# Kernel optimization log

Hardware: AMD Instinct MI355X
Metric: run time of the kernel (lower is better)

The kernel has to match this reference:

```python
import jax, jax.numpy as jnp
import numpy as np

D_MODEL = 1024
NUM_HEADS = 16
HEAD_DIM = D_MODEL // NUM_HEADS


def setup_inputs() -> dict:
    key = jax.random.key(0)
    k_x, k_wqkv, k_bqkv, k_wfc, k_bfc = jax.random.split(key, 5)
    scale_in = 1.0 / np.sqrt(D_MODEL)
    return {
        "x": jax.random.normal(k_x, (2, 2048, D_MODEL), dtype=jnp.float32),
        # torch nn.Linear stores weight as [out_features, in_features]
        "w_qkv": jax.random.uniform(k_wqkv, (3 * D_MODEL, D_MODEL), jnp.float32, -scale_in, scale_in),
        "b_qkv": jax.random.uniform(k_bqkv, (3 * D_MODEL,), jnp.float32, -scale_in, scale_in),
        "w_fc": jax.random.uniform(k_wfc, (D_MODEL, D_MODEL), jnp.float32, -scale_in, scale_in),
        "b_fc": jax.random.uniform(k_bfc, (D_MODEL,), jnp.float32, -scale_in, scale_in),
    }


def reference(x, w_qkv, b_qkv, w_fc, b_fc):
    B, S, _ = x.shape
    # fused QKV projection: [B,S,3*d_model]
    qkv = jnp.einsum("bsd,ed->bse", x, w_qkv) + b_qkv
    # [B,S,H,3*head_dim] -> [B,H,S,3*head_dim]
    qkv = qkv.reshape(B, S, NUM_HEADS, 3 * HEAD_DIM).transpose(0, 2, 1, 3)
    Q, K, V = jnp.split(qkv, 3, axis=-1)  # each [B,H,S,head_dim]
    scores = jnp.einsum("bhqd,bhkd->bhqk", Q, K) / np.sqrt(HEAD_DIM).astype(np.float32)
    attention = jax.nn.softmax(scores, axis=-1)  # [B,H,S,S]
    values = jnp.einsum("bhqk,bhkd->bhqd", attention, V)
    # [B,H,S,head_dim] -> [B,S,d_model]
    values = values.transpose(0, 2, 1, 3).reshape(B, S, D_MODEL)
    out = jnp.einsum("bsd,ed->bse", values, w_fc) + b_fc
    return out
```

## Files before the change

kernel.cpp:

```cpp
#include <hip/hip_runtime.h>
#include <hip/hip_bf16.h>
#include <hip/hip_fp16.h>

#define D_MODEL 1024
#define NH 16
#define HD 64
#define BATCH 2
#define SEQ 2048

typedef __attribute__((ext_vector_type(8))) short short8;
typedef __attribute__((ext_vector_type(4))) float floatx4;
typedef __attribute__((ext_vector_type(16))) float floatx16;
typedef __attribute__((ext_vector_type(8))) _Float16 half8;

static __device__ __forceinline__ short f2bf(float f) {
    __hip_bfloat16 h = __float2bfloat16(f);
    return *reinterpret_cast<short*>(&h);
}
static __device__ __forceinline__ unsigned int pk2bf(float a, float b) {
    float2 t; t.x = a; t.y = b;
    __hip_bfloat162 h2 = __float22bfloat162_rn(t);
    return *reinterpret_cast<unsigned int*>(&h2);
}
static __device__ __forceinline__ void pl32swap(unsigned &a, unsigned &b) {
    asm("v_permlane32_swap_b32 %0, %1" : "+v"(a), "+v"(b));
}
static __device__ __forceinline__ short8 mk8(unsigned a, unsigned b,
                                             unsigned c, unsigned d) {
    union { unsigned u[4]; short8 s; } t;
    t.u[0] = a; t.u[1] = b; t.u[2] = c; t.u[3] = d;
    return t.s;
}
static __device__ __forceinline__ float fexp2(float x) {
    return __builtin_amdgcn_exp2f(x);
}

#define GLDS(gp, lp) __builtin_amdgcn_global_load_lds( \
    (const __attribute__((address_space(1))) void*)(gp), \
    (__attribute__((address_space(3))) void*)(lp), 16, 0, 0)

__global__ __launch_bounds__(256) void cvt_all(
    const float* __restrict__ x, const float* __restrict__ wq,
    const float* __restrict__ wf,
    short* __restrict__ Xb, short* __restrict__ Wqb, short* __restrict__ Wfb)
{
    int i = blockIdx.x * 256 + threadIdx.x;
    const float* src; short* dst; int off;
    if (i < 524288)      { src = x;  dst = Xb;  off = i; }
    else if (i < 917504) { src = wq; dst = Wqb; off = i - 524288; }
    else                 { src = wf; dst = Wfb; off = i - 917504; }
    float4 a = *reinterpret_cast<const float4*>(src + off * 8);
    float4 b = *reinterpret_cast<const float4*>(src + off * 8 + 4);
    short8 o;
    o[0] = f2bf(a.x); o[1] = f2bf(a.y); o[2] = f2bf(a.z); o[3] = f2bf(a.w);
    o[4] = f2bf(b.x); o[5] = f2bf(b.y); o[6] = f2bf(b.z); o[7] = f2bf(b.w);
    *reinterpret_cast<short8*>(dst + off * 8) = o;
}

__global__ __launch_bounds__(256) void qkv_gemm(
    const short* __restrict__ X, const short* __restrict__ W,
    const float* __restrict__ bias,
    short* __restrict__ Qs, short* __restrict__ Ks, short* __restrict__ Vt_g)
{
    __shared__ __align__(16) short SH[4][128 * 32];
    const int tid = threadIdx.x;

    const int lin = blockIdx.x;
    const int g = lin & 7;
    const int loc = lin >> 3;
    const int mi = loc / 3;
    const int j3 = loc - mi * 3;
    const int m0 = mi * 128;
    const int n0 = (g + 8 * j3) * 128;
    const int bi = m0 >> 11, sl0 = m0 & 2047;

    const int w = tid >> 6, lane = tid & 63;
    const int quad = lane >> 4, l15 = lane & 15;
    const int wm2 = w >> 1, wn2 = w & 1;

    const int r1 = tid >> 2,        c1 = tid & 3;
    const int g1 = c1 ^ (r1 & 3) ^ ((r1 >> 2) & 3);
    const int r2 = (tid + 256) >> 2, c2 = tid & 3;
    const int g2 = c2 ^ (r2 & 3) ^ ((r2 >> 2) & 3);

    const short* Xs1 = X + (size_t)(m0 + r1) * 1024 + g1 * 8;
    const short* Xs2 = X + (size_t)(m0 + r2) * 1024 + g2 * 8;
    const short* Ws1 = W + (size_t)(n0 + r1) * 1024 + g1 * 8;
    const short* Ws2 = W + (size_t)(n0 + r2) * 1024 + g2 * 8;

    const int rsw = (quad ^ (l15 & 3) ^ ((l15 >> 2) & 3)) * 8;

    floatx4 acc[4][4];
#pragma unroll
    for (int i = 0; i < 4; i++)
#pragma unroll
        for (int j = 0; j < 4; j++) acc[i][j] = (floatx4)0.0f;

    GLDS(Xs1, &SH[0][tid * 8]);
    GLDS(Xs2, &SH[0][(tid + 256) * 8]);
    GLDS(Ws1, &SH[2][tid * 8]);
    GLDS(Ws2, &SH[2][(tid + 256) * 8]);
    __syncthreads();

    int cur = 0;
    for (int step = 0; step < 32; step++) {
        const int kn = (step + 1) * 32;
        GLDS(Xs1 + kn, &SH[cur ^ 1][tid * 8]);
        GLDS(Xs2 + kn, &SH[cur ^ 1][(tid + 256) * 8]);
        GLDS(Ws1 + kn, &SH[2 + (cur ^ 1)][tid * 8]);
        GLDS(Ws2 + kn, &SH[2 + (cur ^ 1)][(tid + 256) * 8]);

        const short* As = &SH[cur][0];
        const short* Bs = &SH[2 + cur][0];
        short8 a[4], b[4];
#pragma unroll
        for (int t = 0; t < 4; t++) {
            int ra = wm2 * 64 + t * 16 + l15;
            int rb = wn2 * 64 + t * 16 + l15;
            a[t] = *reinterpret_cast<const short8*>(&As[ra * 32 + rsw]);
            b[t] = *reinterpret_cast<const short8*>(&Bs[rb * 32 + rsw]);
        }
#pragma unroll
        for (int mt = 0; mt < 4; mt++)
#pragma unroll
            for (int nt = 0; nt < 4; nt++)
                acc[mt][nt] = __builtin_amdgcn_mfma_f32_16x16x32_bf16(
                    a[mt], b[nt], acc[mt][nt], 0, 0, 0);

        __syncthreads();
        cur ^= 1;
    }

    __syncthreads();
    short* EA = &SH[0][0];
    short* T  = &SH[0][0];
#pragma unroll
    for (int half = 0; half < 2; half++) {
        const int colg0 = n0 + half * 64;
        const int h = colg0 / 192;
        const int t = (colg0 % 192) / 64;
        if (wn2 == half) {
#pragma unroll
            for (int nt = 0; nt < 4; nt++) {
                int jj = nt * 16 + l15;
                float bv = bias[colg0 + jj];
#pragma unroll
                for (int mt = 0; mt < 4; mt++) {
#pragma unroll
                    for (int r = 0; r < 4; r++) {
                        int ml = wm2 * 64 + mt * 16 + quad * 4 + r;
                        float v = acc[mt][nt][r] + bv;
                        if (t == 0) v *= 0.18033688f;
                        if (t < 2) EA[ml * 72 + jj] = f2bf(v);
                        else       T[jj * 136 + ml] = f2bf(v);
                    }
                }
            }
        }
        __syncthreads();
        if (t < 2) {
            short* dst = (t == 0) ? Qs : Ks;
#pragma unroll
            for (int i = 0; i < 4; i++) {
                int c = tid + i * 256;
                int row = c >> 3, ck = c & 7;
                uint4 u = *reinterpret_cast<const uint4*>(&EA[row * 72 + ck * 8]);
                *reinterpret_cast<uint4*>(
                    &dst[((size_t)(bi * NH + h) * SEQ + sl0 + row) * HD + ck * 8]) = u;
            }
        } else {
#pragma unroll
            for (int i = 0; i < 4; i++) {
                int c = tid + i * 256;
                int d = c >> 4, ck = c & 15;
                uint4 u = *reinterpret_cast<const uint4*>(&T[d * 136 + ck * 8]);
                *reinterpret_cast<uint4*>(
                    &Vt_g[((size_t)(bi * NH + h) * HD + d) * SEQ + sl0 + ck * 8]) = u;
            }
        }
        __syncthreads();
    }
}

__global__ __launch_bounds__(512, 4) void attn_kernel(
    const short* __restrict__ Qs, const short* __restrict__ Ks,
    const short* __restrict__ Vt_g,
    _Float16* __restrict__ Opart, float* __restrict__ lpart)
{
    __shared__ __align__(16) short Kl[2][32 * 64];
    __shared__ __align__(16) short Vl[2][32 * 64];

    const int tid = threadIdx.x;
    const int w = tid >> 6;
    const int lane = tid & 63;
    const int hi = lane >> 5, l31 = lane & 31;

    const int lin = blockIdx.x;
    const int xcd = lin & 7;
    const int j = lin >> 3;
    const int qb = j & 7;
    const int grp = xcd + 8 * (j >> 3);
    const int khalf = grp & 1;
    const int h = (grp >> 1) & 15;
    const int bi = grp >> 5;
    const int bh = bi * NH + h;
    const int kbase = bh * SEQ * HD;
    const int vbase = bh * HD * SEQ;
    const int kt0 = khalf * (SEQ / 2);
    const int qw = qb * 256 + w * 32;

    const int st = tid & 255;
    const int sr = st >> 3;
    const int ss = st & 7;
    const int cgs = ss ^ (sr & 7);
    const short* kg = Ks + kbase + (size_t)(kt0 + sr) * HD + cgs * 8;
    const short* vg = Vt_g + vbase +
                      (size_t)(sr + (cgs >> 2) * 32) * SEQ + kt0 + (cgs & 3) * 8;

    const short8 onesv = {(short)0x3F80, (short)0x3F80, (short)0x3F80, (short)0x3F80,
                          (short)0x3F80, (short)0x3F80, (short)0x3F80, (short)0x3F80};

    short8 aq[4];
    {
        const short* qp = Qs + kbase + (size_t)(qw + l31) * HD + hi * 8;
#pragma unroll
        for (int c = 0; c < 4; c++)
            aq[c] = *reinterpret_cast<const short8*>(qp + c * 16);
    }

    floatx16 o0 = (floatx16)0.0f, o1 = (floatx16)0.0f, ol = (floatx16)0.0f;

    const int rbase = (l31 >> 3) * 512 + (l31 & 7) * 64;
    const int rx = l31 & 7;

    if (tid < 256) GLDS(kg, &Kl[0][st * 8]);
    else           GLDS(vg, &Vl[0][st * 8]);
    __syncthreads();

    int cur = 0;
    for (int it = 0; it < SEQ / 2 / 32; it++) {
        if (tid < 256) GLDS(kg + (size_t)(it + 1) * (32 * HD), &Kl[cur ^ 1][st * 8]);
        else           GLDS(vg + (it + 1) * 32, &Vl[cur ^ 1][st * 8]);

        const short* Kb = &Kl[cur][0];
        const short* Vb = &Vl[cur][0];
        short8 kf[4], vA0, vA1, vB0, vB1;
#pragma unroll
        for (int c = 0; c < 4; c++)
            kf[c] = *reinterpret_cast<const short8*>(
                Kb + rbase + (((2 * c + hi) ^ rx) * 8));
        vA0 = *reinterpret_cast<const short8*>(Vb + rbase + (((0 + hi) ^ rx) * 8));
        vA1 = *reinterpret_cast<const short8*>(Vb + rbase + (((2 + hi) ^ rx) * 8));
        vB0 = *reinterpret_cast<const short8*>(Vb + rbase + (((4 + hi) ^ rx) * 8));
        vB1 = *reinterpret_cast<const short8*>(Vb + rbase + (((6 + hi) ^ rx) * 8));

        floatx16 s = (floatx16)0.0f;
        s = __builtin_amdgcn_mfma_f32_32x32x16_bf16(kf[0], aq[0], s, 0, 0, 0);
        s = __builtin_amdgcn_mfma_f32_32x32x16_bf16(kf[1], aq[1], s, 0, 0, 0);
        s = __builtin_amdgcn_mfma_f32_32x32x16_bf16(kf[2], aq[2], s, 0, 0, 0);
        s = __builtin_amdgcn_mfma_f32_32x32x16_bf16(kf[3], aq[3], s, 0, 0, 0);

        float p[16];
#pragma unroll
        for (int r = 0; r < 16; r++) p[r] = fexp2(s[r]);

        unsigned d0a = pk2bf(p[0], p[1]),   d2a = pk2bf(p[4], p[5]);
        unsigned d1a = pk2bf(p[2], p[3]),   d3a = pk2bf(p[6], p[7]);
        pl32swap(d0a, d2a);
        pl32swap(d1a, d3a);
        unsigned d0b = pk2bf(p[8], p[9]),   d2b = pk2bf(p[12], p[13]);
        unsigned d1b = pk2bf(p[10], p[11]), d3b = pk2bf(p[14], p[15]);
        pl32swap(d0b, d2b);
        pl32swap(d1b, d3b);
        short8 pa0 = mk8(d0a, d1a, d2a, d3a);
        short8 pa1 = mk8(d0b, d1b, d2b, d3b);

        o0 = __builtin_amdgcn_mfma_f32_32x32x16_bf16(pa0, vA0, o0, 0, 0, 0);
        o1 = __builtin_amdgcn_mfma_f32_32x32x16_bf16(pa0, vB0, o1, 0, 0, 0);
        o0 = __builtin_amdgcn_mfma_f32_32x32x16_bf16(pa1, vA1, o0, 0, 0, 0);
        o1 = __builtin_amdgcn_mfma_f32_32x32x16_bf16(pa1, vB1, o1, 0, 0, 0);
        ol = __builtin_amdgcn_mfma_f32_32x32x16_bf16(pa0, onesv, ol, 0, 0, 0);
        ol = __builtin_amdgcn_mfma_f32_32x32x16_bf16(pa1, onesv, ol, 0, 0, 0);

        __syncthreads();
        cur ^= 1;
    }

#pragma unroll
    for (int r = 0; r < 16; r++) {
        int ql = qw + (r & 3) + 8 * (r >> 2) + 4 * hi;
        size_t base = (size_t)khalf * (4096u * 1024u) +
                      ((size_t)bi * SEQ + ql) * D_MODEL + h * HD;
        Opart[base + l31]      = (_Float16)o0[r];
        Opart[base + 32 + l31] = (_Float16)o1[r];
        if (l31 == 0)
            lpart[khalf * 65536 + bh * SEQ + ql] = ol[r];
    }
}

__global__ __launch_bounds__(256) void combine_kernel(
    const _Float16* __restrict__ O, const float* __restrict__ lp,
    short* __restrict__ attnb)
{
    int i = blockIdx.x * 256 + threadIdx.x;
    int m = i >> 7;
    int e0 = (i & 127) * 8;
    int bi = m >> 11, s = m & 2047, h = e0 >> 6;
    int bh = bi * NH + h;
    float l = lp[bh * SEQ + s] + lp[65536 + bh * SEQ + s];
    float rl = 1.0f / l;
    size_t off = (size_t)m * D_MODEL + e0;
    half8 a = *reinterpret_cast<const half8*>(O + off);
    half8 b = *reinterpret_cast<const half8*>(O + 4096u * 1024u + off);
    short8 out;
#pragma unroll
    for (int j = 0; j < 8; j++)
        out[j] = f2bf(((float)a[j] + (float)b[j]) * rl);
    *reinterpret_cast<short8*>(attnb + off) = out;
}

__global__ __launch_bounds__(256) void fc_gemm(
    const short* __restrict__ A, const short* __restrict__ W,
    const float* __restrict__ bias, float* __restrict__ out)
{
    __shared__ __align__(16) short As[128 * 64];
    __shared__ __align__(16) short Bs[64 * 64];
    const int tid = threadIdx.x;
    const int m0 = blockIdx.y * 128;
    const int n0 = blockIdx.x * 64;
    const int w = tid >> 6, lane = tid & 63;
    const int quad = lane >> 4, l15 = lane & 15;
    const int wm2 = w >> 1, wn2 = w & 1;

    const int rg = lane >> 3;
    const int sl = lane & 7;
    const int cg = sl ^ rg;

    floatx4 acc[4][2];
#pragma unroll
    for (int i = 0; i < 4; i++)
#pragma unroll
        for (int j = 0; j < 2; j++) acc[i][j] = (floatx4)0.0f;

    for (int k0 = 0; k0 < 1024; k0 += 64) {
        __syncthreads();
#pragma unroll
        for (int j = 0; j < 4; j++) {
            int g = w * 4 + j;
            int r = g * 8 + rg;
            GLDS(&A[(size_t)(m0 + r) * 1024 + k0 + cg * 8], &As[g * 512]);
        }
#pragma unroll
        for (int j = 0; j < 2; j++) {
            int g = w * 2 + j;
            int r = g * 8 + rg;
            GLDS(&W[(size_t)(n0 + r) * 1024 + k0 + cg * 8], &Bs[g * 512]);
        }
        __syncthreads();
#pragma unroll
        for (int kk = 0; kk < 2; kk++) {
            int swz = ((kk * 4 + quad) ^ (l15 & 7)) * 8;
            short8 a[4], b[2];
#pragma unroll
            for (int i = 0; i < 4; i++)
                a[i] = *reinterpret_cast<const short8*>(
                    &As[(wm2 * 64 + i * 16 + l15) * 64 + swz]);
#pragma unroll
            for (int j = 0; j < 2; j++)
                b[j] = *reinterpret_cast<const short8*>(
                    &Bs[(wn2 * 32 + j * 16 + l15) * 64 + swz]);
#pragma unroll
            for (int mt = 0; mt < 4; mt++)
#pragma unroll
                for (int nt = 0; nt < 2; nt++)
                    acc[mt][nt] = __builtin_amdgcn_mfma_f32_16x16x32_bf16(
                        a[mt], b[nt], acc[mt][nt], 0, 0, 0);
        }
    }

#pragma unroll
    for (int nt = 0; nt < 2; nt++) {
        int col = n0 + wn2 * 32 + nt * 16 + l15;
        float bv = bias[col];
#pragma unroll
        for (int mt = 0; mt < 4; mt++) {
#pragma unroll
            for (int r = 0; r < 4; r++) {
                int row = m0 + wm2 * 64 + mt * 16 + quad * 4 + r;
                out[row * 1024 + col] = acc[mt][nt][r] + bv;
            }
        }
    }
}

extern "C" void kernel_launch(void* const* d_in, const int* in_sizes, int n_in,
                              void* d_out, int out_size, void* d_ws, size_t ws_size,
                              hipStream_t stream) {
    const float* x     = (const float*)d_in[0];
    const float* w_qkv = (const float*)d_in[1];
    const float* b_qkv = (const float*)d_in[2];
    const float* w_fc  = (const float*)d_in[3];
    const float* b_fc  = (const float*)d_in[4];
    float* out = (float*)d_out;

    const size_t M1 = 1024u * 1024u;
    short* ws = (short*)d_ws;
    short* Qs    = ws;
    short* Ks    = ws + 4 * M1;
    short* Vt_g  = ws + 8 * M1;
    short* Wfb   = ws + 12 * M1;
    short* Xb    = ws + 13 * M1;
    short* Wqb   = ws + 17 * M1;
    _Float16* Opart = (_Float16*)(ws + 13 * M1);
    float* lpart = (float*)(ws + 21 * M1);
    short* attnb = Qs;

    cvt_all<<<4096, 256, 0, stream>>>(x, w_qkv, w_fc, Xb, Wqb, Wfb);
    qkv_gemm<<<768, 256, 0, stream>>>(Xb, Wqb, b_qkv, Qs, Ks, Vt_g);
    attn_kernel<<<512, 512, 0, stream>>>(Qs, Ks, Vt_g, Opart, lpart);
    combine_kernel<<<2048, 256, 0, stream>>>(Opart, lpart, attnb);
    fc_gemm<<<dim3(16, 32), 256, 0, stream>>>(attnb, Wfb, b_fc, out);
}
```

Measured before the change: 188.4 us.

## Double-buffer the FC GEMM shared-memory tiles with a K-step of 32

Result: slower. 194.8 us (+3.4%).

```diff
diff --git a/kernel.cpp b/kernel.cpp
--- a/kernel.cpp
+++ b/kernel.cpp
@@ -323,8 +323,8 @@
     const short* __restrict__ A, const short* __restrict__ W,
     const float* __restrict__ bias, float* __restrict__ out)
 {
-    __shared__ __align__(16) short As[128 * 64];
-    __shared__ __align__(16) short Bs[64 * 64];
+    __shared__ __align__(16) short SA[2][128 * 32];
+    __shared__ __align__(16) short SB[2][64 * 32];
     const int tid = threadIdx.x;
     const int m0 = blockIdx.y * 128;
     const int n0 = blockIdx.x * 64;
@@ -332,9 +332,16 @@
     const int quad = lane >> 4, l15 = lane & 15;
     const int wm2 = w >> 1, wn2 = w & 1;
 
-    const int rg = lane >> 3;
-    const int sl = lane & 7;
-    const int cg = sl ^ rg;
+    const int r1 = tid >> 2,         c1 = tid & 3;
+    const int g1 = c1 ^ (r1 & 3) ^ ((r1 >> 2) & 3);
+    const int r2 = (tid + 256) >> 2, c2 = tid & 3;
+    const int g2 = c2 ^ (r2 & 3) ^ ((r2 >> 2) & 3);
+
+    const short* As1 = A + (size_t)(m0 + r1) * 1024 + g1 * 8;
+    const short* As2 = A + (size_t)(m0 + r2) * 1024 + g2 * 8;
+    const short* Bs1 = W + (size_t)(n0 + r1) * 1024 + g1 * 8;
+
+    const int rsw = (quad ^ (l15 & 3) ^ ((l15 >> 2) & 3)) * 8;
 
     floatx4 acc[4][2];
 #pragma unroll
@@ -342,40 +349,40 @@
 #pragma unroll
         for (int j = 0; j < 2; j++) acc[i][j] = (floatx4)0.0f;
 
-    for (int k0 = 0; k0 < 1024; k0 += 64) {
+    GLDS(As1, &SA[0][tid * 8]);
+    GLDS(As2, &SA[0][(tid + 256) * 8]);
+    GLDS(Bs1, &SB[0][tid * 8]);
+    __syncthreads();
+
+    int cur = 0;
+    for (int step = 0; step < 32; step++) {
+        const int kn = (step + 1) * 32;
+        GLDS(As1 + kn, &SA[cur ^ 1][tid * 8]);
+        GLDS(As2 + kn, &SA[cur ^ 1][(tid + 256) * 8]);
+        GLDS(Bs1 + kn, &SB[cur ^ 1][tid * 8]);
+
+        const short* Ab = &SA[cur][0];
+        const short* Bb = &SB[cur][0];
+        short8 a[4], b[2];
+#pragma unroll
+        for (int i = 0; i < 4; i++) {
+            int ra = wm2 * 64 + i * 16 + l15;
+            a[i] = *reinterpret_cast<const short8*>(&Ab[ra * 32 + rsw]);
+        }
+#pragma unroll
+        for (int j = 0; j < 2; j++) {
+            int rb = wn2 * 32 + j * 16 + l15;
+            b[j] = *reinterpret_cast<const short8*>(&Bb[rb * 32 + rsw]);
+        }
+#pragma unroll
+        for (int mt = 0; mt < 4; mt++)
+#pragma unroll
+            for (int nt = 0; nt < 2; nt++)
+                acc[mt][nt] = __builtin_amdgcn_mfma_f32_16x16x32_bf16(
+                    a[mt], b[nt], acc[mt][nt], 0, 0, 0);
+
         __syncthreads();
-#pragma unroll
-        for (int j = 0; j < 4; j++) {
-            int g = w * 4 + j;
-            int r = g * 8 + rg;
-            GLDS(&A[(size_t)(m0 + r) * 1024 + k0 + cg * 8], &As[g * 512]);
-        }
-#pragma unroll
-        for (int j = 0; j < 2; j++) {
-            int g = w * 2 + j;
-            int r = g * 8 + rg;
-            GLDS(&W[(size_t)(n0 + r) * 1024 + k0 + cg * 8], &Bs[g * 512]);
-        }
-        __syncthreads();
-#pragma unroll
-        for (int kk = 0; kk < 2; kk++) {
-            int swz = ((kk * 4 + quad) ^ (l15 & 7)) * 8;
-            short8 a[4], b[2];
-#pragma unroll
-            for (int i = 0; i < 4; i++)
-                a[i] = *reinterpret_cast<const short8*>(
-                    &As[(wm2 * 64 + i * 16 + l15) * 64 + swz]);
-#pragma unroll
-            for (int j = 0; j < 2; j++)
-                b[j] = *reinterpret_cast<const short8*>(
-                    &Bs[(wn2 * 32 + j * 16 + l15) * 64 + swz]);
-#pragma unroll
-            for (int mt = 0; mt < 4; mt++)
-#pragma unroll
-                for (int nt = 0; nt < 2; nt++)
-                    acc[mt][nt] = __builtin_amdgcn_mfma_f32_16x16x32_bf16(
-                        a[mt], b[nt], acc[mt][nt], 0, 0, 0);
-        }
+        cur ^= 1;
     }
 
 #pragma unroll
```
